# Performance work log

Hardware: AMD Instinct MI355X
Metric: run time of the kernel (lower is better)

## Reference

```python
import jax, jax.numpy as jnp
import numpy as np

B, S, D = 8, 4096, 512
EPS = 1e-6


def setup_inputs() -> dict:
    key = jax.random.key(0)
    ks = jax.random.split(key, 9)
    scale = 1.0 / np.sqrt(D)
    inp = {
        "x_seq": jax.random.normal(ks[0], (B, S, D), dtype=jnp.float32),
        "Wq": jax.random.uniform(ks[1], (D, D), jnp.float32, -scale, scale),
        "bq": jax.random.uniform(ks[2], (D,), jnp.float32, -scale, scale),
        "Wk": jax.random.uniform(ks[3], (D, D), jnp.float32, -scale, scale),
        "bk": jax.random.uniform(ks[4], (D,), jnp.float32, -scale, scale),
        "Wv": jax.random.uniform(ks[5], (D, D), jnp.float32, -scale, scale),
        "bv": jax.random.uniform(ks[6], (D,), jnp.float32, -scale, scale),
        "Wa": jax.random.uniform(ks[7], (D, D), jnp.float32, -scale, scale),
        "ba": jax.random.uniform(ks[8], (D,), jnp.float32, -scale, scale),
    }
    return inp


def _forward(x_seq, Wq, bq, Wk, bk, Wv, bv, Wa, ba):
    # Precompute all projections for the whole sequence (big GEMMs).
    q = jax.nn.relu(jnp.einsum('bsd,ed->bse', x_seq, Wq) + bq)  # phi = relu
    k = jax.nn.relu(jnp.einsum('bsd,ed->bse', x_seq, Wk) + bk)
    v = jnp.einsum('bsd,ed->bse', x_seq, Wv) + bv
    a = jax.nn.sigmoid(jnp.einsum('bsd,ed->bse', x_seq, Wa) + ba)

    # time-major for scan: (S, B, D)
    qs, ks_, vs, as_ = (jnp.swapaxes(t, 0, 1) for t in (q, k, v, a))

    def step(carry, inp):
        s, z = carry                      # s: (B,D,D), z: (B,D)
        q_t, k_t, v_t, a_t = inp
        s = a_t[:, :, None] * s + k_t[:, :, None] * v_t[:, None, :]
        z = a_t * z + k_t
        num = jnp.einsum('bi,bij->bj', q_t, s)
        den = jnp.sum(q_t * z, axis=-1, keepdims=True) + EPS
        return (s, z), num / den

    s0 = jnp.zeros((x_seq.shape[0], x_seq.shape[2], x_seq.shape[2]), x_seq.dtype)
    z0 = jnp.zeros((x_seq.shape[0], x_seq.shape[2]), x_seq.dtype)
    _, ys = jax.lax.scan(step, (s0, z0), (qs, ks_, vs, as_))
    return jnp.swapaxes(ys, 0, 1)  # (B, S, D)


def reference(x_seq, Wq, bq, Wk, bk, Wv, bv, Wa, ba):
    return _forward(x_seq, Wq, bq, Wk, bk, Wv, bv, Wa, ba)
```

## Files before the change

kernel.cpp:

```cpp
#include <hip/hip_runtime.h>
#include <hip/hip_bf16.h>
#include <cstdint>
#include <cstddef>

#define D_DIM 512
#define B_DIM 8
#define S_DIM 4096
#define M_DIM (B_DIM * S_DIM)
#define CHUNK 64
#define NCHUNK (S_DIM / CHUNK)
#define NSEG 8
#define CSEG (NCHUNK / NSEG)
#define EPS_C 1e-6f

typedef __attribute__((ext_vector_type(8))) short bf16x8;
typedef __attribute__((ext_vector_type(4))) float f32x4;

__device__ __forceinline__ unsigned short f2bf(float f) {
  uint32_t u = __float_as_uint(f);
  u = (u + 0x7fffu + ((u >> 16) & 1u)) >> 16;
  return (unsigned short)u;
}
__device__ __forceinline__ float bf2f(unsigned short s) { return __uint_as_float(((uint32_t)s) << 16); }

__global__ void cvt_f32_bf16(const float* __restrict__ in, unsigned short* __restrict__ out, int n4) {
  int i = blockIdx.x * blockDim.x + threadIdx.x;
  int stride = gridDim.x * blockDim.x;
  for (; i < n4; i += stride) {
    float4 f = ((const float4*)in)[i];
    ushort4 o;
    o.x = f2bf(f.x); o.y = f2bf(f.y); o.z = f2bf(f.z); o.w = f2bf(f.w);
    ((ushort4*)out)[i] = o;
  }
}

#define TM 128
#define TN 128
#define BK 32

__global__ __launch_bounds__(256) void proj_gemm(
    const unsigned short* __restrict__ Xb,
    const unsigned short* __restrict__ Wb,
    const float* __restrict__ bq, const float* __restrict__ bk,
    const float* __restrict__ bv, const float* __restrict__ ba,
    unsigned short* __restrict__ q_ws, unsigned short* __restrict__ k_ws,
    unsigned short* __restrict__ v_ws, unsigned short* __restrict__ g_ws) {
  __shared__ unsigned short SB[TM * BK + TN * BK];
  unsigned short* As = SB;
  unsigned short* Bs = SB + TM * BK;

  const int proj = blockIdx.z;
  const unsigned short* W = Wb + (size_t)proj * D_DIM * D_DIM;
  const int m0 = blockIdx.x * TM;
  const int n0 = blockIdx.y * TN;
  const int tid = threadIdx.x;
  const int lane = tid & 63;
  const int wave = tid >> 6;
  const int wm = (wave & 1) * 64;
  const int wn = (wave >> 1) * 64;
  const int quad = lane >> 4;
  const int l16 = lane & 15;

  f32x4 acc[4][4];
#pragma unroll
  for (int i = 0; i < 4; ++i)
#pragma unroll
    for (int j = 0; j < 4; ++j) acc[i][j] = (f32x4){0.f, 0.f, 0.f, 0.f};

  const int rw = lane >> 2;
  const int kq = (lane & 3) * 8;

  for (int kc = 0; kc < D_DIM; kc += BK) {
    __syncthreads();
    {
      const unsigned short* gA0 = &Xb[(size_t)(m0 + wave * 16 + rw) * D_DIM + kc + kq];
      const unsigned short* gA1 = &Xb[(size_t)(m0 + 64 + wave * 16 + rw) * D_DIM + kc + kq];
      const unsigned short* gB0 = &W[(size_t)(n0 + wave * 16 + rw) * D_DIM + kc + kq];
      const unsigned short* gB1 = &W[(size_t)(n0 + 64 + wave * 16 + rw) * D_DIM + kc + kq];
      __builtin_amdgcn_global_load_lds(
          (const __attribute__((address_space(1))) void*)gA0,
          (__attribute__((address_space(3))) void*)&As[(wave * 16) * BK], 16, 0, 0);
      __builtin_amdgcn_global_load_lds(
          (const __attribute__((address_space(1))) void*)gA1,
          (__attribute__((address_space(3))) void*)&As[(64 + wave * 16) * BK], 16, 0, 0);
      __builtin_amdgcn_global_load_lds(
          (const __attribute__((address_space(1))) void*)gB0,
          (__attribute__((address_space(3))) void*)&Bs[(wave * 16) * BK], 16, 0, 0);
      __builtin_amdgcn_global_load_lds(
          (const __attribute__((address_space(1))) void*)gB1,
          (__attribute__((address_space(3))) void*)&Bs[(64 + wave * 16) * BK], 16, 0, 0);
    }
    __syncthreads();

    bf16x8 afr[4], bfr[4];
#pragma unroll
    for (int im = 0; im < 4; ++im)
      afr[im] = *(const bf16x8*)&As[(wm + im * 16 + l16) * BK + quad * 8];
#pragma unroll
    for (int in = 0; in < 4; ++in)
      bfr[in] = *(const bf16x8*)&Bs[(wn + in * 16 + l16) * BK + quad * 8];
#pragma unroll
    for (int im = 0; im < 4; ++im)
#pragma unroll
      for (int in = 0; in < 4; ++in)
        acc[im][in] = __builtin_amdgcn_mfma_f32_16x16x32_bf16(afr[im], bfr[in], acc[im][in], 0, 0, 0);
  }

  __syncthreads();

  const float* bias = (proj == 0) ? bq : (proj == 1) ? bk : (proj == 2) ? bv : ba;
  unsigned short* outp = (proj == 0) ? q_ws : (proj == 1) ? k_ws : (proj == 2) ? v_ws : g_ws;
  const bool do_relu = (proj <= 1);
  unsigned short* EP = &SB[wave * 64 * 32];

#pragma unroll
  for (int p = 0; p < 2; ++p) {
#pragma unroll
    for (int half = 0; half < 2; ++half) {
      const int in = 2 * p + half;
      const int nn = n0 + wn + in * 16 + l16;
      const float bn = bias[nn];
#pragma unroll
      for (int im = 0; im < 4; ++im) {
#pragma unroll
        for (int vv = 0; vv < 4; ++vv) {
          float val = acc[im][in][vv] + bn;
          if (do_relu) val = fmaxf(val, 0.f);
          EP[(im * 16 + quad * 4 + vv) * 32 + half * 16 + l16] = f2bf(val);
        }
      }
    }
#pragma unroll
    for (int it = 0; it < 4; ++it) {
      const int row = it * 16 + (lane >> 2);
      const int ccol = (lane & 3) * 8;
      bf16x8 vdat = *(const bf16x8*)&EP[row * 32 + ccol];
      size_t gidx = (size_t)(m0 + wm + row) * D_DIM + (size_t)(n0 + wn + p * 32 + ccol);
      *(bf16x8*)&outp[gidx] = vdat;
    }
  }
}

__global__ __launch_bounds__(512) void prep(
    const unsigned short* __restrict__ q, const unsigned short* __restrict__ k,
    const unsigned short* __restrict__ g,
    unsigned short* __restrict__ qt, unsigned short* __restrict__ kt,
    unsigned short* __restrict__ kh,
    float* __restrict__ Af, float* __restrict__ khs) {
  __shared__ float segp[8][512];
  const int c = blockIdx.x, b = blockIdx.y;
  const int seg = threadIdx.x >> 6;
  const int t = threadIdx.x & 63;
  const int i0 = t * 8;
  const int r0 = seg * 8;
  const size_t t0 = (size_t)b * S_DIM + (size_t)c * CHUNK;
  const size_t cb = ((size_t)b * NCHUNK + c) * D_DIM;

  float sp[8];
#pragma unroll
  for (int j = 0; j < 8; ++j) sp[j] = 1.f;
  for (int r = 0; r < 8; ++r) {
    bf16x8 gv = *(const bf16x8*)&g[(t0 + r0 + r) * D_DIM + i0];
#pragma unroll
    for (int j = 0; j < 8; ++j)
      sp[j] *= 1.f / (1.f + __expf(-bf2f((unsigned short)gv[j])));
  }
  *(float4*)&segp[seg][i0] = *(float4*)&sp[0];
  *(float4*)&segp[seg][i0 + 4] = *(float4*)&sp[4];
  __syncthreads();

  float pre[8], tot[8];
#pragma unroll
  for (int j = 0; j < 8; ++j) { pre[j] = 1.f; tot[j] = 1.f; }
  for (int s2 = 0; s2 < 8; ++s2) {
    float4 v0 = *(const float4*)&segp[s2][i0];
    float4 v1 = *(const float4*)&segp[s2][i0 + 4];
    float v[8] = {v0.x, v0.y, v0.z, v0.w, v1.x, v1.y, v1.z, v1.w};
#pragma unroll
    for (int j = 0; j < 8; ++j) {
      tot[j] *= v[j];
      if (s2 < seg) pre[j] *= v[j];
    }
  }
  if (seg == 0) {
    float4 a0 = {tot[0], tot[1], tot[2], tot[3]};
    float4 a1 = {tot[4], tot[5], tot[6], tot[7]};
    *(float4*)&Af[cb + i0] = a0;
    *(float4*)&Af[cb + i0 + 4] = a1;
  }

  float cum[8], ssum[8];
#pragma unroll
  for (int j = 0; j < 8; ++j) { cum[j] = pre[j]; ssum[j] = 0.f; }
  for (int r = 0; r < 8; ++r) {
    size_t idx = (t0 + r0 + r) * D_DIM + i0;
    bf16x8 gv = *(const bf16x8*)&g[idx];
    bf16x8 qv8 = *(const bf16x8*)&q[idx];
    bf16x8 kv8 = *(const bf16x8*)&k[idx];
    bf16x8 oq, ok, okh;
#pragma unroll
    for (int j = 0; j < 8; ++j) {
      cum[j] *= 1.f / (1.f + __expf(-bf2f((unsigned short)gv[j])));
      float qv = bf2f((unsigned short)qv8[j]);
      float kv = bf2f((unsigned short)kv8[j]);
      oq[j] = (short)f2bf(qv * cum[j]);
      float inv = 1.f / cum[j];
      ok[j] = (short)f2bf(kv * inv);
      float khf = kv * (tot[j] * inv);
      okh[j] = (short)f2bf(khf);
      ssum[j] += khf;
    }
    *(bf16x8*)&qt[idx] = oq;
    *(bf16x8*)&kt[idx] = ok;
    *(bf16x8*)&kh[idx] = okh;
  }

  __syncthreads();
  *(float4*)&segp[seg][i0] = *(float4*)&ssum[0];
  *(float4*)&segp[seg][i0 + 4] = *(float4*)&ssum[4];
  __syncthreads();
  if (seg == 0) {
    float s[8];
#pragma unroll
    for (int j = 0; j < 8; ++j) s[j] = 0.f;
    for (int s2 = 0; s2 < 8; ++s2) {
      float4 v0 = *(const float4*)&segp[s2][i0];
      float4 v1 = *(const float4*)&segp[s2][i0 + 4];
      s[0] += v0.x; s[1] += v0.y; s[2] += v0.z; s[3] += v0.w;
      s[4] += v1.x; s[5] += v1.y; s[6] += v1.z; s[7] += v1.w;
    }
    float4 a0 = {s[0], s[1], s[2], s[3]};
    float4 a1 = {s[4], s[5], s[6], s[7]};
    *(float4*)&khs[cb + i0] = a0;
    *(float4*)&khs[cb + i0 + 4] = a1;
  }
}

__global__ __launch_bounds__(256) void transpose_cd(
    const unsigned short* __restrict__ in, unsigned short* __restrict__ outT) {
  __shared__ unsigned short tile[CHUNK][264];
  const int c = blockIdx.x, b = blockIdx.y;
  const size_t base_in = ((size_t)b * S_DIM + (size_t)c * CHUNK) * D_DIM;
  const size_t base_out = ((size_t)b * NCHUNK + c) * (size_t)D_DIM * CHUNK;
  const int tid = threadIdx.x;
#pragma unroll
  for (int h = 0; h < 2; ++h) {
    if (h) __syncthreads();
#pragma unroll
    for (int it = 0; it < 8; ++it) {
      int flat = (it * 256 + tid) * 8;
      int row = flat >> 8;
      int col = flat & 255;
      *(uint4*)&tile[row][col] = *(const uint4*)&in[base_in + (size_t)row * D_DIM + h * 256 + col];
    }
    __syncthreads();
#pragma unroll
    for (int it = 0; it < 8; ++it) {
      int wq = it * 256 + tid;
      int i_loc = wq >> 3;
      int r0 = (wq & 7) * 8;
      ushort4 v0, v1;
      v0.x = tile[r0 + 0][i_loc]; v0.y = tile[r0 + 1][i_loc];
      v0.z = tile[r0 + 2][i_loc]; v0.w = tile[r0 + 3][i_loc];
      v1.x = tile[r0 + 4][i_loc]; v1.y = tile[r0 + 5][i_loc];
      v1.z = tile[r0 + 6][i_loc]; v1.w = tile[r0 + 7][i_loc];
      size_t o = base_out + (size_t)(h * 256 + i_loc) * CHUNK + r0;
      *(ushort4*)&outT[o] = v0;
      *(ushort4*)&outT[o + 4] = v1;
    }
  }
}

__global__ __launch_bounds__(256) void intra(
    const unsigned short* __restrict__ qt, const unsigned short* kt,
    const unsigned short* __restrict__ VT,
    unsigned short* numI, float* __restrict__ rs) {
  __shared__ unsigned short P_lds[CHUNK][CHUNK + 8];
  const int c = blockIdx.x, b = blockIdx.y;
  const size_t t0 = (size_t)b * S_DIM + (size_t)c * CHUNK;
  const int lane = threadIdx.x & 63, w = threadIdx.x >> 6;
  const int l16 = lane & 15, q4 = lane >> 4;

  f32x4 accP[4];
#pragma unroll
  for (int n = 0; n < 4; ++n) accP[n] = (f32x4){0.f, 0.f, 0.f, 0.f};
#pragma unroll
  for (int ks = 0; ks < 16; ++ks) {
    bf16x8 afr = *(const bf16x8*)&qt[(t0 + 16 * w + l16) * D_DIM + 32 * ks + 8 * q4];
#pragma unroll
    for (int n = 0; n < 4; ++n) {
      bf16x8 bfr = *(const bf16x8*)&kt[(t0 + 16 * n + l16) * D_DIM + 32 * ks + 8 * q4];
      accP[n] = __builtin_amdgcn_mfma_f32_16x16x32_bf16(afr, bfr, accP[n], 0, 0, 0);
    }
  }
  float rsum[4] = {0.f, 0.f, 0.f, 0.f};
#pragma unroll
  for (int n = 0; n < 4; ++n) {
    int m = 16 * n + l16;
#pragma unroll
    for (int vv = 0; vv < 4; ++vv) {
      int r = 16 * w + 4 * q4 + vv;
      float pv = (m <= r) ? accP[n][vv] : 0.f;
      rsum[vv] += pv;
      P_lds[r][m] = f2bf(pv);
    }
  }
#pragma unroll
  for (int msk = 1; msk < 16; msk <<= 1) {
#pragma unroll
    for (int vv = 0; vv < 4; ++vv) rsum[vv] += __shfl_xor(rsum[vv], msk, 64);
  }
  if (l16 == 0) {
#pragma unroll
    for (int vv = 0; vv < 4; ++vv) rs[t0 + 16 * w + 4 * q4 + vv] = rsum[vv];
  }
  __syncthreads();
  bf16x8 pa0 = *(const bf16x8*)&P_lds[16 * w + l16][8 * q4];
  bf16x8 pa1 = *(const bf16x8*)&P_lds[16 * w + l16][32 + 8 * q4];
  const size_t vtb = ((size_t)b * NCHUNK + c) * (size_t)D_DIM * CHUNK;
#pragma unroll 4
  for (int nt = 0; nt < 32; ++nt) {
    bf16x8 b0 = *(const bf16x8*)&VT[vtb + (size_t)(nt * 16 + l16) * CHUNK + 8 * q4];
    bf16x8 b1 = *(const bf16x8*)&VT[vtb + (size_t)(nt * 16 + l16) * CHUNK + 32 + 8 * q4];
    f32x4 acc = (f32x4){0.f, 0.f, 0.f, 0.f};
    acc = __builtin_amdgcn_mfma_f32_16x16x32_bf16(pa0, b0, acc, 0, 0, 0);
    acc = __builtin_amdgcn_mfma_f32_16x16x32_bf16(pa1, b1, acc, 0, 0, 0);
#pragma unroll
    for (int vv = 0; vv < 4; ++vv)
      numI[(t0 + 16 * w + 4 * q4 + vv) * D_DIM + nt * 16 + l16] = f2bf(acc[vv]);
  }
}

__global__ __launch_bounds__(512) void zscan(
    const float* __restrict__ Af, const float* __restrict__ khs,
    float* __restrict__ zall, float* __restrict__ Pseg) {
  const int b = blockIdx.x;
  const int i = threadIdx.x;
  float z = 0.f, rp = 1.f;
  for (int c = 0; c < NCHUNK; ++c) {
    const size_t cb = ((size_t)b * NCHUNK + c) * D_DIM;
    zall[cb + i] = z;
    float af = Af[cb + i];
    z = fmaf(af, z, khs[cb + i]);
    rp *= af;
    if ((c & (CSEG - 1)) == CSEG - 1) {
      Pseg[((size_t)b * NSEG + (c / CSEG)) * D_DIM + i] = rp;
      rp = 1.f;
    }
  }
}

__global__ __launch_bounds__(512) void denk(
    const unsigned short* __restrict__ qt, const float* __restrict__ zall,
    float* rs_invden) {
  const int c = blockIdx.x, b = blockIdx.y;
  const int lane = threadIdx.x & 63, w = threadIdx.x >> 6;
  const size_t t0 = (size_t)b * S_DIM + (size_t)c * CHUNK;
  const size_t zb = ((size_t)b * NCHUNK + c) * D_DIM;
  float4 z0 = *(const float4*)&zall[zb + lane * 8];
  float4 z1 = *(const float4*)&zall[zb + lane * 8 + 4];
#pragma unroll
  for (int rr = 0; rr < 8; ++rr) {
    int r = 8 * w + rr;
    bf16x8 qv = *(const bf16x8*)&qt[(t0 + r) * D_DIM + lane * 8];
    float p = 0.f;
    p = fmaf(bf2f((unsigned short)qv[0]), z0.x, p);
    p = fmaf(bf2f((unsigned short)qv[1]), z0.y, p);
    p = fmaf(bf2f((unsigned short)qv[2]), z0.z, p);
    p = fmaf(bf2f((unsigned short)qv[3]), z0.w, p);
    p = fmaf(bf2f((unsigned short)qv[4]), z1.x, p);
    p = fmaf(bf2f((unsigned short)qv[5]), z1.y, p);
    p = fmaf(bf2f((unsigned short)qv[6]), z1.z, p);
    p = fmaf(bf2f((unsigned short)qv[7]), z1.w, p);
#pragma unroll
    for (int msk = 1; msk < 64; msk <<= 1) p += __shfl_xor(p, msk, 64);
    if (lane == 0) {
      float* iv = &rs_invden[t0 + r];
      *iv = 1.f / (p + *iv + EPS_C);
    }
  }
}

__global__ __launch_bounds__(512, 2) void useg_k(
    const unsigned short* __restrict__ khT, const unsigned short* __restrict__ VT,
    const float* __restrict__ Af, unsigned short* __restrict__ U) {
  const int s = blockIdx.x, jt = blockIdx.y, b = blockIdx.z;
  const int lane = threadIdx.x & 63, w = threadIdx.x >> 6;
  const int l16 = lane & 15, q4 = lane >> 4;
  const int j0 = jt * 128;
  const int iw = 128 * (w & 3);
  const int jw = 64 * (w >> 2);

  f32x4 acc[8][4];
#pragma unroll
  for (int T = 0; T < 8; ++T)
#pragma unroll
    for (int h = 0; h < 4; ++h) acc[T][h] = (f32x4){0.f, 0.f, 0.f, 0.f};

  for (int cc = 0; cc < CSEG; ++cc) {
    const int c = s * CSEG + cc;
    const size_t cb = ((size_t)b * NCHUNK + c) * D_DIM;
    const size_t ob = cb * CHUNK;
#pragma unroll
    for (int T = 0; T < 8; ++T) {
      float4 af = *(const float4*)&Af[cb + iw + 16 * T + 4 * q4];
#pragma unroll
      for (int h = 0; h < 4; ++h) {
        acc[T][h][0] *= af.x; acc[T][h][1] *= af.y; acc[T][h][2] *= af.z; acc[T][h][3] *= af.w;
      }
    }
    bf16x8 bv0[4], bv1[4];
#pragma unroll
    for (int h = 0; h < 4; ++h) {
      bv0[h] = *(const bf16x8*)&VT[ob + (size_t)(j0 + jw + 16 * h + l16) * CHUNK + 8 * q4];
      bv1[h] = *(const bf16x8*)&VT[ob + (size_t)(j0 + jw + 16 * h + l16) * CHUNK + 32 + 8 * q4];
    }
#pragma unroll
    for (int T = 0; T < 8; ++T) {
      bf16x8 a0 = *(const bf16x8*)&khT[ob + (size_t)(iw + 16 * T + l16) * CHUNK + 8 * q4];
      bf16x8 a1 = *(const bf16x8*)&khT[ob + (size_t)(iw + 16 * T + l16) * CHUNK + 32 + 8 * q4];
#pragma unroll
      for (int h = 0; h < 4; ++h) {
        acc[T][h] = __builtin_amdgcn_mfma_f32_16x16x32_bf16(a0, bv0[h], acc[T][h], 0, 0, 0);
        acc[T][h] = __builtin_amdgcn_mfma_f32_16x16x32_bf16(a1, bv1[h], acc[T][h], 0, 0, 0);
      }
    }
  }
  const size_t ub = ((size_t)b * NSEG + s) * D_DIM;
#pragma unroll
  for (int T = 0; T < 8; ++T)
#pragma unroll
    for (int h = 0; h < 4; ++h) {
      uint2 pk;
      pk.x = (uint32_t)f2bf(acc[T][h][0]) | ((uint32_t)f2bf(acc[T][h][1]) << 16);
      pk.y = (uint32_t)f2bf(acc[T][h][2]) | ((uint32_t)f2bf(acc[T][h][3]) << 16);
      *(uint2*)&U[(ub + j0 + jw + 16 * h + l16) * (size_t)D_DIM + iw + 16 * T + 4 * q4] = pk;
    }
}

__global__ __launch_bounds__(256) void sscan(
    const float* __restrict__ Pseg, unsigned short* __restrict__ U) {
  const int b = blockIdx.y;
  const int flat = blockIdx.x * 256 + threadIdx.x;
  const int j = flat >> 6;
  const int i0 = (flat & 63) * 8;
  float acc[8];
#pragma unroll
  for (int t = 0; t < 8; ++t) acc[t] = 0.f;
  for (int s = 0; s < NSEG; ++s) {
    const size_t pb = ((size_t)b * NSEG + s) * D_DIM;
    unsigned short* up = &U[(pb + j) * (size_t)D_DIM + i0];
    uint4 u = *(const uint4*)up;
    float4 p0 = *(const float4*)&Pseg[pb + i0];
    float4 p1 = *(const float4*)&Pseg[pb + i0 + 4];
    float uv[8];
    uv[0] = bf2f((unsigned short)(u.x & 0xffff)); uv[1] = bf2f((unsigned short)(u.x >> 16));
    uv[2] = bf2f((unsigned short)(u.y & 0xffff)); uv[3] = bf2f((unsigned short)(u.y >> 16));
    uv[4] = bf2f((unsigned short)(u.z & 0xffff)); uv[5] = bf2f((unsigned short)(u.z >> 16));
    uv[6] = bf2f((unsigned short)(u.w & 0xffff)); uv[7] = bf2f((unsigned short)(u.w >> 16));
    uint4 o;
    o.x = (uint32_t)f2bf(acc[0]) | ((uint32_t)f2bf(acc[1]) << 16);
    o.y = (uint32_t)f2bf(acc[2]) | ((uint32_t)f2bf(acc[3]) << 16);
    o.z = (uint32_t)f2bf(acc[4]) | ((uint32_t)f2bf(acc[5]) << 16);
    o.w = (uint32_t)f2bf(acc[6]) | ((uint32_t)f2bf(acc[7]) << 16);
    *(uint4*)up = o;
    acc[0] = fmaf(p0.x, acc[0], uv[0]);
    acc[1] = fmaf(p0.y, acc[1], uv[1]);
    acc[2] = fmaf(p0.z, acc[2], uv[2]);
    acc[3] = fmaf(p0.w, acc[3], uv[3]);
    acc[4] = fmaf(p1.x, acc[4], uv[4]);
    acc[5] = fmaf(p1.y, acc[5], uv[5]);
    acc[6] = fmaf(p1.z, acc[6], uv[6]);
    acc[7] = fmaf(p1.w, acc[7], uv[7]);
  }
}

__global__ __launch_bounds__(512, 2) void scan2(
    const unsigned short* __restrict__ qt, const unsigned short* __restrict__ khT,
    const unsigned short* __restrict__ VT, const float* __restrict__ Af,
    const unsigned short* __restrict__ Sin,
    const unsigned short* __restrict__ numI, const float* __restrict__ invden,
    float* __restrict__ out) {
  __shared__ unsigned short STj[128][520];
  const int s = blockIdx.x, jt = blockIdx.y, b = blockIdx.z;
  const int lane = threadIdx.x & 63, w = threadIdx.x >> 6;
  const int l16 = lane & 15, q4 = lane >> 4;
  const int j0 = jt * 128;
  const int iw = 128 * (w & 3);
  const int jw = 64 * (w >> 2);
  const int rw = 16 * (w & 3);
  const int jo = 64 * (w >> 2);

  f32x4 acc[8][4];

  {
    const size_t pb = ((size_t)b * NSEG + s) * D_DIM;
#pragma unroll
    for (int T = 0; T < 8; ++T)
#pragma unroll
      for (int h = 0; h < 4; ++h) {
        uint2 uu = *(const uint2*)&Sin[(pb + j0 + jw + 16 * h + l16) * (size_t)D_DIM + iw + 16 * T + 4 * q4];
        acc[T][h][0] = bf2f((unsigned short)(uu.x & 0xffff));
        acc[T][h][1] = bf2f((unsigned short)(uu.x >> 16));
        acc[T][h][2] = bf2f((unsigned short)(uu.y & 0xffff));
        acc[T][h][3] = bf2f((unsigned short)(uu.y >> 16));
      }
  }

  for (int cc = 0; cc < CSEG; ++cc) {
    const int c = s * CSEG + cc;
    const size_t cb = ((size_t)b * NCHUNK + c) * D_DIM;
    const size_t t0 = (size_t)b * S_DIM + (size_t)c * CHUNK;
    const size_t ob = cb * CHUNK;

#pragma unroll
    for (int T = 0; T < 8; ++T)
#pragma unroll
      for (int h = 0; h < 4; ++h) {
        uint2 pk;
        pk.x = (uint32_t)f2bf(acc[T][h][0]) | ((uint32_t)f2bf(acc[T][h][1]) << 16);
        pk.y = (uint32_t)f2bf(acc[T][h][2]) | ((uint32_t)f2bf(acc[T][h][3]) << 16);
        *(uint2*)&STj[jw + 16 * h + l16][iw + 16 * T + 4 * q4] = pk;
      }
    __syncthreads();

    {
      f32x4 accO[4];
#pragma unroll
      for (int h = 0; h < 4; ++h) accO[h] = (f32x4){0.f, 0.f, 0.f, 0.f};
#pragma unroll
      for (int ks = 0; ks < 16; ++ks) {
        bf16x8 afr = *(const bf16x8*)&qt[(t0 + rw + l16) * D_DIM + 32 * ks + 8 * q4];
#pragma unroll
        for (int h = 0; h < 4; ++h) {
          bf16x8 bfr = *(const bf16x8*)&STj[jo + 16 * h + l16][32 * ks + 8 * q4];
          accO[h] = __builtin_amdgcn_mfma_f32_16x16x32_bf16(afr, bfr, accO[h], 0, 0, 0);
        }
      }
#pragma unroll
      for (int h = 0; h < 4; ++h)
#pragma unroll
        for (int vv = 0; vv < 4; ++vv) {
          size_t t = t0 + rw + 4 * q4 + vv;
          int j = j0 + jo + 16 * h + l16;
          float idv = invden[t];
          float nI = bf2f(numI[t * D_DIM + j]);
          out[t * D_DIM + j] = (accO[h][vv] + nI) * idv;
        }
    }

    if (cc != CSEG - 1) {
#pragma unroll
      for (int T = 0; T < 8; ++T) {
        float4 af = *(const float4*)&Af[cb + iw + 16 * T + 4 * q4];
#pragma unroll
        for (int h = 0; h < 4; ++h) {
          acc[T][h][0] *= af.x; acc[T][h][1] *= af.y; acc[T][h][2] *= af.z; acc[T][h][3] *= af.w;
        }
      }
      bf16x8 bv0[4], bv1[4];
#pragma unroll
      for (int h = 0; h < 4; ++h) {
        bv0[h] = *(const bf16x8*)&VT[ob + (size_t)(j0 + jw + 16 * h + l16) * CHUNK + 8 * q4];
        bv1[h] = *(const bf16x8*)&VT[ob + (size_t)(j0 + jw + 16 * h + l16) * CHUNK + 32 + 8 * q4];
      }
#pragma unroll
      for (int T = 0; T < 8; ++T) {
        bf16x8 a0 = *(const bf16x8*)&khT[ob + (size_t)(iw + 16 * T + l16) * CHUNK + 8 * q4];
        bf16x8 a1 = *(const bf16x8*)&khT[ob + (size_t)(iw + 16 * T + l16) * CHUNK + 32 + 8 * q4];
#pragma unroll
        for (int h = 0; h < 4; ++h) {
          acc[T][h] = __builtin_amdgcn_mfma_f32_16x16x32_bf16(a0, bv0[h], acc[T][h], 0, 0, 0);
          acc[T][h] = __builtin_amdgcn_mfma_f32_16x16x32_bf16(a1, bv1[h], acc[T][h], 0, 0, 0);
        }
      }
    }
    __syncthreads();
  }
}

extern "C" void kernel_launch(void* const* d_in, const int* in_sizes, int n_in,
                              void* d_out, int out_size, void* d_ws, size_t ws_size,
                              hipStream_t stream) {
  const float* x  = (const float*)d_in[0];
  const float* Wq = (const float*)d_in[1];
  const float* bq = (const float*)d_in[2];
  const float* Wk = (const float*)d_in[3];
  const float* bk = (const float*)d_in[4];
  const float* Wv = (const float*)d_in[5];
  const float* bv = (const float*)d_in[6];
  const float* Wa = (const float*)d_in[7];
  const float* ba = (const float*)d_in[8];
  float* out = (float*)d_out;

  const size_t MD2 = (size_t)M_DIM * D_DIM * 2;
  uint8_t* w = (uint8_t*)d_ws;
  unsigned short* xb   = (unsigned short*)w; w += MD2;
  unsigned short* wb   = (unsigned short*)w; w += (size_t)4 * D_DIM * D_DIM * 2;
  unsigned short* q_ws = (unsigned short*)w; w += MD2;
  unsigned short* k_ws = (unsigned short*)w; w += MD2;
  unsigned short* v_ws = (unsigned short*)w; w += MD2;
  unsigned short* g_ws = (unsigned short*)w; w += MD2;
  float* Af     = (float*)w; w += (size_t)B_DIM * NCHUNK * D_DIM * 4;
  float* khs    = (float*)w; w += (size_t)B_DIM * NCHUNK * D_DIM * 4;
  float* invden = (float*)w; w += (size_t)M_DIM * 4;

  unsigned short* qt   = xb;
  unsigned short* kt   = q_ws;
  unsigned short* kh   = k_ws;
  unsigned short* VT   = g_ws;
  unsigned short* khT  = v_ws;
  unsigned short* numI = q_ws;
  unsigned short* U    = k_ws;
  float* zall = (float*)wb;
  float* Pseg = (float*)((uint8_t*)wb + (1 << 20));

  cvt_f32_bf16<<<1024, 256, 0, stream>>>(x, xb, M_DIM * D_DIM / 4);
  cvt_f32_bf16<<<128, 256, 0, stream>>>(Wq, wb + 0 * D_DIM * D_DIM, D_DIM * D_DIM / 4);
  cvt_f32_bf16<<<128, 256, 0, stream>>>(Wk, wb + 1 * D_DIM * D_DIM, D_DIM * D_DIM / 4);
  cvt_f32_bf16<<<128, 256, 0, stream>>>(Wv, wb + 2 * D_DIM * D_DIM, D_DIM * D_DIM / 4);
  cvt_f32_bf16<<<128, 256, 0, stream>>>(Wa, wb + 3 * D_DIM * D_DIM, D_DIM * D_DIM / 4);

  proj_gemm<<<dim3(M_DIM / TM, D_DIM / TN, 4), 256, 0, stream>>>(
      xb, wb, bq, bk, bv, ba, q_ws, k_ws, v_ws, g_ws);

  prep<<<dim3(NCHUNK, B_DIM), 512, 0, stream>>>(q_ws, k_ws, g_ws, qt, kt, kh, Af, khs);
  transpose_cd<<<dim3(NCHUNK, B_DIM), 256, 0, stream>>>(v_ws, VT);
  transpose_cd<<<dim3(NCHUNK, B_DIM), 256, 0, stream>>>(kh, khT);
  zscan<<<B_DIM, 512, 0, stream>>>(Af, khs, zall, Pseg);
  intra<<<dim3(NCHUNK, B_DIM), 256, 0, stream>>>(qt, kt, VT, numI, invden);
  denk<<<dim3(NCHUNK, B_DIM), 512, 0, stream>>>(qt, zall, invden);
  useg_k<<<dim3(NSEG, 4, B_DIM), 512, 0, stream>>>(khT, VT, Af, U);
  sscan<<<dim3(128, B_DIM), 256, 0, stream>>>(Pseg, U);
  scan2<<<dim3(NSEG, 4, B_DIM), 512, 0, stream>>>(qt, khT, VT, Af, U, numI, invden, out);
}
```

Baseline: 530.7 us.

## Stage V chunks in swizzled LDS and retile state update per wave

```diff
diff --git a/kernel.cpp b/kernel.cpp
--- a/kernel.cpp
+++ b/kernel.cpp
@@ -15,6 +15,11 @@
 
 typedef __attribute__((ext_vector_type(8))) short bf16x8;
 typedef __attribute__((ext_vector_type(4))) float f32x4;
+
+#define GLOAD_LDS16(src, dst)                                              \
+  __builtin_amdgcn_global_load_lds(                                        \
+      (const __attribute__((address_space(1))) void*)(src),                \
+      (__attribute__((address_space(3))) void*)(dst), 16, 0, 0)
 
 __device__ __forceinline__ unsigned short f2bf(float f) {
   uint32_t u = __float_as_uint(f);
@@ -77,18 +82,10 @@
       const unsigned short* gA1 = &Xb[(size_t)(m0 + 64 + wave * 16 + rw) * D_DIM + kc + kq];
       const unsigned short* gB0 = &W[(size_t)(n0 + wave * 16 + rw) * D_DIM + kc + kq];
       const unsigned short* gB1 = &W[(size_t)(n0 + 64 + wave * 16 + rw) * D_DIM + kc + kq];
-      __builtin_amdgcn_global_load_lds(
-          (const __attribute__((address_space(1))) void*)gA0,
-          (__attribute__((address_space(3))) void*)&As[(wave * 16) * BK], 16, 0, 0);
-      __builtin_amdgcn_global_load_lds(
-          (const __attribute__((address_space(1))) void*)gA1,
-          (__attribute__((address_space(3))) void*)&As[(64 + wave * 16) * BK], 16, 0, 0);
-      __builtin_amdgcn_global_load_lds(
-          (const __attribute__((address_space(1))) void*)gB0,
-          (__attribute__((address_space(3))) void*)&Bs[(wave * 16) * BK], 16, 0, 0);
-      __builtin_amdgcn_global_load_lds(
-          (const __attribute__((address_space(1))) void*)gB1,
-          (__attribute__((address_space(3))) void*)&Bs[(64 + wave * 16) * BK], 16, 0, 0);
+      GLOAD_LDS16(gA0, &As[(wave * 16) * BK]);
+      GLOAD_LDS16(gA1, &As[(64 + wave * 16) * BK]);
+      GLOAD_LDS16(gB0, &Bs[(wave * 16) * BK]);
+      GLOAD_LDS16(gB1, &Bs[(64 + wave * 16) * BK]);
     }
     __syncthreads();
 
@@ -384,57 +381,92 @@
 __global__ __launch_bounds__(512, 2) void useg_k(
     const unsigned short* __restrict__ khT, const unsigned short* __restrict__ VT,
     const float* __restrict__ Af, unsigned short* __restrict__ U) {
+  __shared__ unsigned short VTl[2][128 * 64];
   const int s = blockIdx.x, jt = blockIdx.y, b = blockIdx.z;
   const int lane = threadIdx.x & 63, w = threadIdx.x >> 6;
   const int l16 = lane & 15, q4 = lane >> 4;
   const int j0 = jt * 128;
-  const int iw = 128 * (w & 3);
-  const int jw = 64 * (w >> 2);
-
-  f32x4 acc[8][4];
-#pragma unroll
-  for (int T = 0; T < 8; ++T)
-#pragma unroll
-    for (int h = 0; h < 4; ++h) acc[T][h] = (f32x4){0.f, 0.f, 0.f, 0.f};
+  const int iw = 64 * w;
+  const int vrow = lane >> 3;
+  const int vswz = (lane & 7) ^ (vrow & 7);
+
+  f32x4 acc[4][8];
+#pragma unroll
+  for (int T = 0; T < 4; ++T)
+#pragma unroll
+    for (int h = 0; h < 8; ++h) acc[T][h] = (f32x4){0.f, 0.f, 0.f, 0.f};
+
+  const size_t cb0 = ((size_t)b * NCHUNK + s * CSEG) * D_DIM;
+  {
+    const size_t ob0 = cb0 * CHUNK;
+#pragma unroll
+    for (int kk = 0; kk < 2; ++kk) {
+      const int k = 2 * w + kk;
+      GLOAD_LDS16(&VT[ob0 + (size_t)(j0 + 8 * k + vrow) * CHUNK + vswz * 8],
+                  &VTl[0][k * 512]);
+    }
+  }
+  bf16x8 a0[4], a1[4];
+  {
+    const size_t ob0 = cb0 * CHUNK;
+#pragma unroll
+    for (int T = 0; T < 4; ++T) {
+      a0[T] = *(const bf16x8*)&khT[ob0 + (size_t)(iw + 16 * T + l16) * CHUNK + 8 * q4];
+      a1[T] = *(const bf16x8*)&khT[ob0 + (size_t)(iw + 16 * T + l16) * CHUNK + 32 + 8 * q4];
+    }
+  }
 
   for (int cc = 0; cc < CSEG; ++cc) {
-    const int c = s * CSEG + cc;
-    const size_t cb = ((size_t)b * NCHUNK + c) * D_DIM;
-    const size_t ob = cb * CHUNK;
-#pragma unroll
-    for (int T = 0; T < 8; ++T) {
+    const size_t cb = cb0 + (size_t)cc * D_DIM;
+    __syncthreads();
+    if (cc + 1 < CSEG) {
+      const size_t obn = (cb + D_DIM) * CHUNK;
+#pragma unroll
+      for (int kk = 0; kk < 2; ++kk) {
+        const int k = 2 * w + kk;
+        GLOAD_LDS16(&VT[obn + (size_t)(j0 + 8 * k + vrow) * CHUNK + vswz * 8],
+                    &VTl[(cc + 1) & 1][k * 512]);
+      }
+    }
+#pragma unroll
+    for (int T = 0; T < 4; ++T) {
       float4 af = *(const float4*)&Af[cb + iw + 16 * T + 4 * q4];
 #pragma unroll
-      for (int h = 0; h < 4; ++h) {
+      for (int h = 0; h < 8; ++h) {
         acc[T][h][0] *= af.x; acc[T][h][1] *= af.y; acc[T][h][2] *= af.z; acc[T][h][3] *= af.w;
       }
     }
-    bf16x8 bv0[4], bv1[4];
-#pragma unroll
-    for (int h = 0; h < 4; ++h) {
-      bv0[h] = *(const bf16x8*)&VT[ob + (size_t)(j0 + jw + 16 * h + l16) * CHUNK + 8 * q4];
-      bv1[h] = *(const bf16x8*)&VT[ob + (size_t)(j0 + jw + 16 * h + l16) * CHUNK + 32 + 8 * q4];
-    }
-#pragma unroll
-    for (int T = 0; T < 8; ++T) {
-      bf16x8 a0 = *(const bf16x8*)&khT[ob + (size_t)(iw + 16 * T + l16) * CHUNK + 8 * q4];
-      bf16x8 a1 = *(const bf16x8*)&khT[ob + (size_t)(iw + 16 * T + l16) * CHUNK + 32 + 8 * q4];
-#pragma unroll
-      for (int h = 0; h < 4; ++h) {
-        acc[T][h] = __builtin_amdgcn_mfma_f32_16x16x32_bf16(a0, bv0[h], acc[T][h], 0, 0, 0);
-        acc[T][h] = __builtin_amdgcn_mfma_f32_16x16x32_bf16(a1, bv1[h], acc[T][h], 0, 0, 0);
+    const unsigned short* Vb = VTl[cc & 1];
+#pragma unroll
+    for (int h = 0; h < 8; ++h) {
+      const int jpos = 16 * h + l16;
+      const int swz = jpos & 7;
+      bf16x8 bv0 = *(const bf16x8*)&Vb[jpos * 64 + ((q4 ^ swz) * 8)];
+      bf16x8 bv1 = *(const bf16x8*)&Vb[jpos * 64 + (((4 + q4) ^ swz) * 8)];
+#pragma unroll
+      for (int T = 0; T < 4; ++T) {
+        acc[T][h] = __builtin_amdgcn_mfma_f32_16x16x32_bf16(a0[T], bv0, acc[T][h], 0, 0, 0);
+        acc[T][h] = __builtin_amdgcn_mfma_f32_16x16x32_bf16(a1[T], bv1, acc[T][h], 0, 0, 0);
+      }
+    }
+    if (cc + 1 < CSEG) {
+      const size_t obn = (cb + D_DIM) * CHUNK;
+#pragma unroll
+      for (int T = 0; T < 4; ++T) {
+        a0[T] = *(const bf16x8*)&khT[obn + (size_t)(iw + 16 * T + l16) * CHUNK + 8 * q4];
+        a1[T] = *(const bf16x8*)&khT[obn + (size_t)(iw + 16 * T + l16) * CHUNK + 32 + 8 * q4];
       }
     }
   }
   const size_t ub = ((size_t)b * NSEG + s) * D_DIM;
 #pragma unroll
-  for (int T = 0; T < 8; ++T)
-#pragma unroll
-    for (int h = 0; h < 4; ++h) {
+  for (int T = 0; T < 4; ++T)
+#pragma unroll
+    for (int h = 0; h < 8; ++h) {
       uint2 pk;
       pk.x = (uint32_t)f2bf(acc[T][h][0]) | ((uint32_t)f2bf(acc[T][h][1]) << 16);
       pk.y = (uint32_t)f2bf(acc[T][h][2]) | ((uint32_t)f2bf(acc[T][h][3]) << 16);
-      *(uint2*)&U[(ub + j0 + jw + 16 * h + l16) * (size_t)D_DIM + iw + 16 * T + 4 * q4] = pk;
+      *(uint2*)&U[(ub + j0 + 16 * h + l16) * (size_t)D_DIM + iw + 16 * T + 4 * q4] = pk;
     }
 }
 
@@ -482,24 +514,26 @@
     const unsigned short* __restrict__ numI, const float* __restrict__ invden,
     float* __restrict__ out) {
   __shared__ unsigned short STj[128][520];
+  __shared__ unsigned short VTl[128 * 64];
   const int s = blockIdx.x, jt = blockIdx.y, b = blockIdx.z;
   const int lane = threadIdx.x & 63, w = threadIdx.x >> 6;
   const int l16 = lane & 15, q4 = lane >> 4;
   const int j0 = jt * 128;
-  const int iw = 128 * (w & 3);
-  const int jw = 64 * (w >> 2);
+  const int iw = 64 * w;
   const int rw = 16 * (w & 3);
   const int jo = 64 * (w >> 2);
-
-  f32x4 acc[8][4];
+  const int vrow = lane >> 3;
+  const int vswz = (lane & 7) ^ (vrow & 7);
+
+  f32x4 acc[4][8];
 
   {
     const size_t pb = ((size_t)b * NSEG + s) * D_DIM;
 #pragma unroll
-    for (int T = 0; T < 8; ++T)
-#pragma unroll
-      for (int h = 0; h < 4; ++h) {
-        uint2 uu = *(const uint2*)&Sin[(pb + j0 + jw + 16 * h + l16) * (size_t)D_DIM + iw + 16 * T + 4 * q4];
+    for (int T = 0; T < 4; ++T)
+#pragma unroll
+      for (int h = 0; h < 8; ++h) {
+        uint2 uu = *(const uint2*)&Sin[(pb + j0 + 16 * h + l16) * (size_t)D_DIM + iw + 16 * T + 4 * q4];
         acc[T][h][0] = bf2f((unsigned short)(uu.x & 0xffff));
         acc[T][h][1] = bf2f((unsigned short)(uu.x >> 16));
         acc[T][h][2] = bf2f((unsigned short)(uu.y & 0xffff));
@@ -512,15 +546,31 @@
     const size_t cb = ((size_t)b * NCHUNK + c) * D_DIM;
     const size_t t0 = (size_t)b * S_DIM + (size_t)c * CHUNK;
     const size_t ob = cb * CHUNK;
-
-#pragma unroll
-    for (int T = 0; T < 8; ++T)
-#pragma unroll
-      for (int h = 0; h < 4; ++h) {
+    const bool upd = (cc != CSEG - 1);
+
+    bf16x8 a0[4], a1[4];
+    if (upd) {
+#pragma unroll
+      for (int kk = 0; kk < 2; ++kk) {
+        const int k = 2 * w + kk;
+        GLOAD_LDS16(&VT[ob + (size_t)(j0 + 8 * k + vrow) * CHUNK + vswz * 8],
+                    &VTl[k * 512]);
+      }
+#pragma unroll
+      for (int T = 0; T < 4; ++T) {
+        a0[T] = *(const bf16x8*)&khT[ob + (size_t)(iw + 16 * T + l16) * CHUNK + 8 * q4];
+        a1[T] = *(const bf16x8*)&khT[ob + (size_t)(iw + 16 * T + l16) * CHUNK + 32 + 8 * q4];
+      }
+    }
+
+#pragma unroll
+    for (int T = 0; T < 4; ++T)
+#pragma unroll
+      for (int h = 0; h < 8; ++h) {
         uint2 pk;
         pk.x = (uint32_t)f2bf(acc[T][h][0]) | ((uint32_t)f2bf(acc[T][h][1]) << 16);
         pk.y = (uint32_t)f2bf(acc[T][h][2]) | ((uint32_t)f2bf(acc[T][h][3]) << 16);
-        *(uint2*)&STj[jw + 16 * h + l16][iw + 16 * T + 4 * q4] = pk;
+        *(uint2*)&STj[16 * h + l16][iw + 16 * T + 4 * q4] = pk;
       }
     __syncthreads();
 
@@ -549,29 +599,25 @@
         }
     }
 
-    if (cc != CSEG - 1) {
-#pragma unroll
-      for (int T = 0; T < 8; ++T) {
+    if (upd) {
+#pragma unroll
+      for (int T = 0; T < 4; ++T) {
         float4 af = *(const float4*)&Af[cb + iw + 16 * T + 4 * q4];
 #pragma unroll
-        for (int h = 0; h < 4; ++h) {
+        for (int h = 0; h < 8; ++h) {
           acc[T][h][0] *= af.x; acc[T][h][1] *= af.y; acc[T][h][2] *= af.z; acc[T][h][3] *= af.w;
         }
       }
-      bf16x8 bv0[4], bv1[4];
-#pragma unroll
-      for (int h = 0; h < 4; ++h) {
-        bv0[h] = *(const bf16x8*)&VT[ob + (size_t)(j0 + jw + 16 * h + l16) * CHUNK + 8 * q4];
-        bv1[h] = *(const bf16x8*)&VT[ob + (size_t)(j0 + jw + 16 * h + l16) * CHUNK + 32 + 8 * q4];
-      }
-#pragma unroll
-      for (int T = 0; T < 8; ++T) {
-        bf16x8 a0 = *(const bf16x8*)&khT[ob + (size_t)(iw + 16 * T + l16) * CHUNK + 8 * q4];
-        bf16x8 a1 = *(const bf16x8*)&khT[ob + (size_t)(iw + 16 * T + l16) * CHUNK + 32 + 8 * q4];
-#pragma unroll
-        for (int h = 0; h < 4; ++h) {
-          acc[T][h] = __builtin_amdgcn_mfma_f32_16x16x32_bf16(a0, bv0[h], acc[T][h], 0, 0, 0);
-          acc[T][h] = __builtin_amdgcn_mfma_f32_16x16x32_bf16(a1, bv1[h], acc[T][h], 0, 0, 0);
+#pragma unroll
+      for (int h = 0; h < 8; ++h) {
+        const int jpos = 16 * h + l16;
+        const int swz = jpos & 7;
+        bf16x8 bv0 = *(const bf16x8*)&VTl[jpos * 64 + ((q4 ^ swz) * 8)];
+        bf16x8 bv1 = *(const bf16x8*)&VTl[jpos * 64 + (((4 + q4) ^ swz) * 8)];
+#pragma unroll
+        for (int T = 0; T < 4; ++T) {
+          acc[T][h] = __builtin_amdgcn_mfma_f32_16x16x32_bf16(a0[T], bv0, acc[T][h], 0, 0, 0);
+          acc[T][h] = __builtin_amdgcn_mfma_f32_16x16x32_bf16(a1[T], bv1, acc[T][h], 0, 0, 0);
         }
       }
     }
```

New measurement: 505.8 us. 1.05x faster.
